# Kernel optimization log

Hardware: AMD Instinct MI355X
Metric: run time of the kernel (lower is better)

The kernel has to match this reference:

```python
import jax, jax.numpy as jnp
import numpy as np

N0, N1, NB = 247808, 22528, 2048
E0, E1 = 225280, 20480
C = 256
EW = 600000

def setup_inputs() -> dict:
    key = jax.random.key(0)
    ks = jax.random.split(key, 16)
    s = 1.0 / np.sqrt(C)
    return {
        "x": jax.random.normal(ks[0], (N0, C), dtype=jnp.float32),
        "src0": jax.random.randint(ks[1], (E0,), 0, N0),
        "dst0": jax.random.randint(ks[2], (E0,), 0, N1),
        "eid0": jax.random.randint(ks[3], (E0,), 0, EW),
        "src1": jax.random.randint(ks[4], (E1,), 0, N1),
        "dst1": jax.random.randint(ks[5], (E1,), 0, NB),
        "eid1": jax.random.randint(ks[6], (E1,), 0, EW),
        "edge_weight": jax.random.uniform(ks[7], (EW,), dtype=jnp.float32),
        "W_rel0": jax.random.uniform(ks[8], (C, C), jnp.float32, -s, s),
        "b0": jax.random.uniform(ks[9], (C,), jnp.float32, -s, s),
        "W_root0": jax.random.uniform(ks[10], (C, C), jnp.float32, -s, s),
        "W_rel1": jax.random.uniform(ks[11], (C, C), jnp.float32, -s, s),
        "b1": jax.random.uniform(ks[12], (C,), jnp.float32, -s, s),
        "W_root1": jax.random.uniform(ks[13], (C, C), jnp.float32, -s, s),
    }

def graph_conv(x, src, dst, ew, n_dst, W_rel, b, W_root):
    # PyG GraphConv, aggr='mean', bipartite: out_i = W_rel * mean_j(e_ji * x_j) + W_root * x_i + b
    msg = ew[:, None] * x[src]                                   # [E, C]
    agg = jax.ops.segment_sum(msg, dst, num_segments=n_dst)      # [n_dst, C]
    cnt = jax.ops.segment_sum(jnp.ones_like(ew), dst, num_segments=n_dst)
    mean = agg / jnp.maximum(cnt, 1.0)[:, None]
    return mean @ W_rel + b + x[:n_dst] @ W_root

def reference(x, src0, dst0, eid0, src1, dst1, eid1, edge_weight,
              W_rel0, b0, W_root0, W_rel1, b1, W_root1):
    h = graph_conv(x, src0, dst0, edge_weight[eid0], N1, W_rel0, b0, W_root0)
    h = jax.nn.relu(h)  # dropout is identity in eval mode
    h = graph_conv(h, src1, dst1, edge_weight[eid1], NB, W_rel1, b1, W_root1)
    return h, jax.nn.log_softmax(h, axis=1)
```

## Files before the change

### kernel.cpp

```cpp
#include <hip/hip_runtime.h>
#include <cstdint>
#include <cmath>

#define N0c 247808
#define N1c 22528
#define NBc 2048
#define E0c 225280
#define E1c 20480
#define Cc  256
#define NDST (N1c + NBc)
#define ETOT (E0c + E1c)

typedef __attribute__((ext_vector_type(8))) short short8;
typedef __attribute__((ext_vector_type(4))) float floatx4;

__device__ inline unsigned short f2bf(float f) {
    union { float f; unsigned u; } cv; cv.f = f;
    unsigned u = cv.u;
    u += 0x7fffu + ((u >> 16) & 1u);
    return (unsigned short)(u >> 16);
}

__global__ __launch_bounds__(256) void prep_kernel(
    const int* __restrict__ dst0, const int* __restrict__ dst1, int* __restrict__ cnt,
    const float* __restrict__ Wrel0, const float* __restrict__ Wroot0,
    const float* __restrict__ Wrel1, const float* __restrict__ Wroot1,
    short* __restrict__ Wp0, short* __restrict__ Wp1) {
    int b = blockIdx.x;
    if (b < ETOT / 256) {
        int e = b * 256 + threadIdx.x;
        if (e < E0c) atomicAdd(&cnt[dst0[e]], 1);
        else         atomicAdd(&cnt[N1c + dst1[e - E0c]], 1);
    } else {
        int gid = (b - ETOT / 256) * 256 + threadIdx.x;
        int lane = gid & 63;
        int kt = (gid >> 6) & 15;
        int nt = (gid >> 10) & 15;
        int layer = gid >> 14;
        const float* Wrel  = layer ? Wrel1  : Wrel0;
        const float* Wroot = layer ? Wroot1 : Wroot0;
        short* Wp = layer ? Wp1 : Wp0;
        int nn = nt * 16 + (lane & 15);
        int kb = kt * 32 + (lane >> 4) * 8;
        short8 v;
#pragma unroll
        for (int j = 0; j < 8; j++) {
            int k = kb + j;
            float f = (k < 256) ? Wrel[k * 256 + nn] : Wroot[(k - 256) * 256 + nn];
            v[j] = (short)f2bf(f);
        }
        *(short8*)(Wp + (((size_t)nt * 16 + kt) * 64 + lane) * 8) = v;
    }
}

__global__ __launch_bounds__(256) void scan_part(const int* __restrict__ in,
                                                 int* __restrict__ out,
                                                 int* __restrict__ partials) {
    __shared__ int wsum[4];
    int t = threadIdx.x, lane = t & 63, w = t >> 6;
    int base = blockIdx.x * 1024 + t * 4;
    int4 v = *(const int4*)(in + base);
    int s = v.x + v.y + v.z + v.w;
    int incl = s;
#pragma unroll
    for (int o = 1; o < 64; o <<= 1) {
        int u = __shfl_up(incl, o);
        if (lane >= o) incl += u;
    }
    if (lane == 63) wsum[w] = incl;
    __syncthreads();
    int woff = 0;
    for (int j = 0; j < w; j++) woff += wsum[j];
    int excl = woff + incl - s;
    int4 o4;
    o4.x = excl; excl += v.x;
    o4.y = excl; excl += v.y;
    o4.z = excl; excl += v.z;
    o4.w = excl; excl += v.w;
    *(int4*)(out + base) = o4;
    if (t == 255) partials[blockIdx.x] = woff + incl;
}

__global__ __launch_bounds__(256) void scan_add(int* __restrict__ off, int* __restrict__ cur,
                                                const int* __restrict__ partials) {
    __shared__ int pfx_s;
    int t = threadIdx.x;
    if (t < 32) {
        int v = (t < NDST / 1024) ? partials[t] : 0;
        int incl = v;
#pragma unroll
        for (int o = 1; o < 32; o <<= 1) {
            int u = __shfl_up(incl, o);
            if (t >= o) incl += u;
        }
        if (t == (int)blockIdx.x) pfx_s = incl - v;
        if (blockIdx.x == 0 && t == NDST / 1024 - 1) off[NDST] = incl;
    }
    __syncthreads();
    int p = pfx_s;
    int base = blockIdx.x * 1024 + t * 4;
    int4 v = *(const int4*)(off + base);
    v.x += p; v.y += p; v.z += p; v.w += p;
    *(int4*)(off + base) = v;
    *(int4*)(cur + base) = v;
}

__global__ void fill_both(const int* __restrict__ src0, const int* __restrict__ dst0,
                          const int* __restrict__ eid0,
                          const int* __restrict__ src1, const int* __restrict__ dst1,
                          const int* __restrict__ eid1,
                          const float* __restrict__ ew,
                          int* __restrict__ cur, int* __restrict__ srcs,
                          float* __restrict__ wsr) {
    int e = blockIdx.x * blockDim.x + threadIdx.x;
    if (e < E0c) {
        int p = atomicAdd(&cur[dst0[e]], 1);
        srcs[p] = src0[e];
        wsr[p] = ew[eid0[e]];
    } else if (e < ETOT) {
        int i = e - E0c;
        int p = atomicAdd(&cur[N1c + dst1[i]], 1);
        srcs[p] = src1[i];
        wsr[p] = ew[eid1[i]];
    }
}

template <bool ROOT>
__global__ __launch_bounds__(256) void gather_mean_bf16(const float* __restrict__ feat,
                                                        const int* __restrict__ off,
                                                        const int* __restrict__ srcs,
                                                        const float* __restrict__ wsr,
                                                        short* __restrict__ outA,
                                                        int baseRow, int nrows) {
    int wid  = (blockIdx.x * blockDim.x + threadIdx.x) >> 6;
    int lane = threadIdx.x & 63;
    if (wid >= nrows) return;
    int crow = baseRow + wid;
    int s = off[crow], e = off[crow + 1];
    float4 acc = make_float4(0.f, 0.f, 0.f, 0.f);
    int i = s;
    for (; i + 3 < e; i += 4) {
        int   s0 = srcs[i],     s1 = srcs[i + 1], s2 = srcs[i + 2], s3 = srcs[i + 3];
        float w0 = wsr[i],      w1 = wsr[i + 1],  w2 = wsr[i + 2],  w3 = wsr[i + 3];
        float4 v0 = ((const float4*)(feat + (size_t)s0 * Cc))[lane];
        float4 v1 = ((const float4*)(feat + (size_t)s1 * Cc))[lane];
        float4 v2 = ((const float4*)(feat + (size_t)s2 * Cc))[lane];
        float4 v3 = ((const float4*)(feat + (size_t)s3 * Cc))[lane];
        acc.x += w0 * v0.x + w1 * v1.x + w2 * v2.x + w3 * v3.x;
        acc.y += w0 * v0.y + w1 * v1.y + w2 * v2.y + w3 * v3.y;
        acc.z += w0 * v0.z + w1 * v1.z + w2 * v2.z + w3 * v3.z;
        acc.w += w0 * v0.w + w1 * v1.w + w2 * v2.w + w3 * v3.w;
    }
    for (; i < e; i++) {
        int sid = srcs[i];
        float w = wsr[i];
        float4 v = ((const float4*)(feat + (size_t)sid * Cc))[lane];
        acc.x += w * v.x; acc.y += w * v.y; acc.z += w * v.z; acc.w += w * v.w;
    }
    float inv = 1.0f / fmaxf((float)(e - s), 1.0f);
    ushort4 o;
    o.x = f2bf(acc.x * inv); o.y = f2bf(acc.y * inv);
    o.z = f2bf(acc.z * inv); o.w = f2bf(acc.w * inv);
    *(ushort4*)(outA + (size_t)wid * 512 + lane * 4) = o;
    if (ROOT) {
        float4 r = ((const float4*)(feat + (size_t)crow * Cc))[lane];
        ushort4 ro;
        ro.x = f2bf(r.x); ro.y = f2bf(r.y); ro.z = f2bf(r.z); ro.w = f2bf(r.w);
        *(ushort4*)(outA + (size_t)wid * 512 + 256 + lane * 4) = ro;
    }
}

template <bool RELU, bool EXTRA, bool SMAX>
__global__ __launch_bounds__(256) void gemm_mfma(const short* __restrict__ A,
                                                 const short* __restrict__ Wp,
                                                 const float* __restrict__ bias,
                                                 float* __restrict__ out,
                                                 short* __restrict__ extra,
                                                 float* __restrict__ out1) {
    __shared__ short As[32 * 520];
    int t = threadIdx.x;
    int base = blockIdx.x * 32;
#pragma unroll
    for (int it = 0; it < 8; it++) {
        int idx = it * 256 + t;
        int row = idx >> 6, c = idx & 63;
        short8 v = *(const short8*)(A + (size_t)(base + row) * 512 + c * 8);
        *(short8*)(&As[row * 520 + c * 8]) = v;
    }
    __syncthreads();

    int lane = t & 63, w = t >> 6;
    int l15 = lane & 15, lq = lane >> 4;
    floatx4 acc[2][4];
#pragma unroll
    for (int rt = 0; rt < 2; rt++)
#pragma unroll
        for (int ct = 0; ct < 4; ct++) acc[rt][ct] = (floatx4){0.f, 0.f, 0.f, 0.f};

    for (int kt = 0; kt < 16; kt++) {
        short8 a0 = *(const short8*)(&As[l15 * 520 + kt * 32 + lq * 8]);
        short8 a1 = *(const short8*)(&As[(16 + l15) * 520 + kt * 32 + lq * 8]);
#pragma unroll
        for (int ct = 0; ct < 4; ct++) {
            int nt = w * 4 + ct;
            short8 b = *(const short8*)(Wp + (((size_t)nt * 16 + kt) * 64 + lane) * 8);
            acc[0][ct] = __builtin_amdgcn_mfma_f32_16x16x32_bf16(a0, b, acc[0][ct], 0, 0, 0);
            acc[1][ct] = __builtin_amdgcn_mfma_f32_16x16x32_bf16(a1, b, acc[1][ct], 0, 0, 0);
        }
    }

    float* Ls = (float*)As;
    if (SMAX) __syncthreads();

#pragma unroll
    for (int rt = 0; rt < 2; rt++)
#pragma unroll
        for (int ct = 0; ct < 4; ct++) {
            int col = (w * 4 + ct) * 16 + l15;
            float bv = bias[col];
#pragma unroll
            for (int r = 0; r < 4; r++) {
                int rl = rt * 16 + lq * 4 + r;
                int row = base + rl;
                float val = acc[rt][ct][r] + bv;
                if (RELU) val = fmaxf(val, 0.f);
                out[(size_t)row * Cc + col] = val;
                if (EXTRA) {
                    if (row < NBc) extra[(size_t)row * 512 + 256 + col] = (short)f2bf(val);
                }
                if (SMAX) Ls[rl * 260 + col] = val;
            }
        }

    if (SMAX) {
        __syncthreads();
        for (int rr = 0; rr < 8; rr++) {
            int rl = w * 8 + rr;
            float4 v = *(const float4*)(Ls + rl * 260 + lane * 4);
            float m = fmaxf(fmaxf(v.x, v.y), fmaxf(v.z, v.w));
#pragma unroll
            for (int o = 32; o; o >>= 1) m = fmaxf(m, __shfl_xor(m, o));
            float s = expf(v.x - m) + expf(v.y - m) + expf(v.z - m) + expf(v.w - m);
#pragma unroll
            for (int o = 32; o; o >>= 1) s += __shfl_xor(s, o);
            float lse = m + logf(s);
            float4 o4;
            o4.x = v.x - lse; o4.y = v.y - lse; o4.z = v.z - lse; o4.w = v.w - lse;
            *(float4*)(out1 + (size_t)(base + rl) * Cc + lane * 4) = o4;
        }
    }
}

extern "C" void kernel_launch(void* const* d_in, const int* in_sizes, int n_in,
                              void* d_out, int out_size, void* d_ws, size_t ws_size,
                              hipStream_t stream) {
    const float* x     = (const float*)d_in[0];
    const int*   src0  = (const int*)d_in[1];
    const int*   dst0  = (const int*)d_in[2];
    const int*   eid0  = (const int*)d_in[3];
    const int*   src1  = (const int*)d_in[4];
    const int*   dst1  = (const int*)d_in[5];
    const int*   eid1  = (const int*)d_in[6];
    const float* ew    = (const float*)d_in[7];
    const float* Wrel0 = (const float*)d_in[8];
    const float* b0    = (const float*)d_in[9];
    const float* Wroot0= (const float*)d_in[10];
    const float* Wrel1 = (const float*)d_in[11];
    const float* b1    = (const float*)d_in[12];
    const float* Wroot1= (const float*)d_in[13];

    char* wsb = (char*)d_ws;
    size_t o = 0;
    auto alloc = [&](size_t bytes) { void* p = wsb + o; o += (bytes + 15) & ~(size_t)15; return p; };
    int*   off   = (int*)  alloc((NDST + 1) * 4);
    int*   cnt   = (int*)  alloc(NDST * 4);
    int*   srcs  = (int*)  alloc(ETOT * 4);
    float* wsr   = (float*)alloc(ETOT * 4);
    int*   parts = (int*)  alloc(64 * 4);
    short* Wp0   = (short*)alloc(16 * 16 * 64 * 8 * 2);
    short* Wp1   = (short*)alloc(16 * 16 * 64 * 8 * 2);
    short* A0    = (short*)alloc((size_t)N1c * 512 * 2);
    short* A1    = (short*)alloc((size_t)NBc * 512 * 2);
    float* h     = (float*)alloc((size_t)N1c * Cc * 4);

    hipMemsetAsync(cnt, 0, NDST * sizeof(int), stream);
    prep_kernel<<<ETOT / 256 + 128, 256, 0, stream>>>(dst0, dst1, cnt,
                                                      Wrel0, Wroot0, Wrel1, Wroot1, Wp0, Wp1);
    scan_part<<<NDST / 1024, 256, 0, stream>>>(cnt, off, parts);
    scan_add<<<NDST / 1024, 256, 0, stream>>>(off, cnt, parts);
    fill_both<<<ETOT / 256, 256, 0, stream>>>(src0, dst0, eid0, src1, dst1, eid1,
                                              ew, cnt, srcs, wsr);

    gather_mean_bf16<true><<<(N1c * 64) / 256, 256, 0, stream>>>(x, off, srcs, wsr, A0, 0, N1c);
    gemm_mfma<true, true, false><<<N1c / 32, 256, 0, stream>>>(A0, Wp0, b0, h, A1, nullptr);

    gather_mean_bf16<false><<<(NBc * 64) / 256, 256, 0, stream>>>(h, off, srcs, wsr, A1, N1c, NBc);
    float* out2 = (float*)d_out;
    gemm_mfma<false, false, true><<<NBc / 32, 256, 0, stream>>>(A1, Wp1, b1, out2, nullptr,
                                                                out2 + (size_t)NBc * Cc);
}
```

Baseline: 442.5 us.

## Fuse neighbor gather-mean into MFMA GEMMs and store hidden layer as bf16

Each layer's gather-mean aggregation and root-row load now write straight into the GEMM's shared-memory A tile, so the bf16 A0/A1 staging buffers and their global round trip are gone. Two kernel launches are removed. The hidden activation is kept only as bf16, which halves the layer-2 gather traffic but makes layer 2 read bf16-rounded h instead of fp32. Edge source and weight are packed into one int2 record so each edge needs one load. The risk is that gather latency inside the GEMM blocks is now serialized with the MFMA phase, with fewer resident blocks available to hide it.

```diff
diff --git a/kernel.cpp b/kernel.cpp
--- a/kernel.cpp
+++ b/kernel.cpp
@@ -19,6 +19,10 @@
     unsigned u = cv.u;
     u += 0x7fffu + ((u >> 16) & 1u);
     return (unsigned short)(u >> 16);
+}
+__device__ inline float bf2f(unsigned short u) {
+    union { unsigned u; float f; } cv; cv.u = ((unsigned)u) << 16;
+    return cv.f;
 }
 
 __global__ __launch_bounds__(256) void prep_kernel(
@@ -110,93 +114,71 @@
                           const int* __restrict__ src1, const int* __restrict__ dst1,
                           const int* __restrict__ eid1,
                           const float* __restrict__ ew,
-                          int* __restrict__ cur, int* __restrict__ srcs,
-                          float* __restrict__ wsr) {
+                          int* __restrict__ cur, int2* __restrict__ recs) {
     int e = blockIdx.x * blockDim.x + threadIdx.x;
     if (e < E0c) {
         int p = atomicAdd(&cur[dst0[e]], 1);
-        srcs[p] = src0[e];
-        wsr[p] = ew[eid0[e]];
+        recs[p] = make_int2(src0[e], __float_as_int(ew[eid0[e]]));
     } else if (e < ETOT) {
         int i = e - E0c;
         int p = atomicAdd(&cur[N1c + dst1[i]], 1);
-        srcs[p] = src1[i];
-        wsr[p] = ew[eid1[i]];
-    }
-}
-
-template <bool ROOT>
-__global__ __launch_bounds__(256) void gather_mean_bf16(const float* __restrict__ feat,
-                                                        const int* __restrict__ off,
-                                                        const int* __restrict__ srcs,
-                                                        const float* __restrict__ wsr,
-                                                        short* __restrict__ outA,
-                                                        int baseRow, int nrows) {
-    int wid  = (blockIdx.x * blockDim.x + threadIdx.x) >> 6;
-    int lane = threadIdx.x & 63;
-    if (wid >= nrows) return;
-    int crow = baseRow + wid;
-    int s = off[crow], e = off[crow + 1];
-    float4 acc = make_float4(0.f, 0.f, 0.f, 0.f);
-    int i = s;
-    for (; i + 3 < e; i += 4) {
-        int   s0 = srcs[i],     s1 = srcs[i + 1], s2 = srcs[i + 2], s3 = srcs[i + 3];
-        float w0 = wsr[i],      w1 = wsr[i + 1],  w2 = wsr[i + 2],  w3 = wsr[i + 3];
-        float4 v0 = ((const float4*)(feat + (size_t)s0 * Cc))[lane];
-        float4 v1 = ((const float4*)(feat + (size_t)s1 * Cc))[lane];
-        float4 v2 = ((const float4*)(feat + (size_t)s2 * Cc))[lane];
-        float4 v3 = ((const float4*)(feat + (size_t)s3 * Cc))[lane];
-        acc.x += w0 * v0.x + w1 * v1.x + w2 * v2.x + w3 * v3.x;
-        acc.y += w0 * v0.y + w1 * v1.y + w2 * v2.y + w3 * v3.y;
-        acc.z += w0 * v0.z + w1 * v1.z + w2 * v2.z + w3 * v3.z;
-        acc.w += w0 * v0.w + w1 * v1.w + w2 * v2.w + w3 * v3.w;
-    }
-    for (; i < e; i++) {
-        int sid = srcs[i];
-        float w = wsr[i];
-        float4 v = ((const float4*)(feat + (size_t)sid * Cc))[lane];
-        acc.x += w * v.x; acc.y += w * v.y; acc.z += w * v.z; acc.w += w * v.w;
-    }
-    float inv = 1.0f / fmaxf((float)(e - s), 1.0f);
-    ushort4 o;
-    o.x = f2bf(acc.x * inv); o.y = f2bf(acc.y * inv);
-    o.z = f2bf(acc.z * inv); o.w = f2bf(acc.w * inv);
-    *(ushort4*)(outA + (size_t)wid * 512 + lane * 4) = o;
-    if (ROOT) {
-        float4 r = ((const float4*)(feat + (size_t)crow * Cc))[lane];
+        recs[p] = make_int2(src1[i], __float_as_int(ew[eid1[i]]));
+    }
+}
+
+__global__ __launch_bounds__(256) void gemm0_fused(const float* __restrict__ x,
+                                                   const int* __restrict__ off,
+                                                   const int2* __restrict__ recs,
+                                                   const short* __restrict__ Wp,
+                                                   const float* __restrict__ bias,
+                                                   short* __restrict__ hb) {
+    __shared__ short As[32 * 520];
+    int t = threadIdx.x, lane = t & 63, w = t >> 6;
+    int base = blockIdx.x * 32;
+
+    for (int r = 0; r < 8; r++) {
+        int rl = w * 8 + r;
+        int row = base + rl;
+        int s = off[row], e = off[row + 1];
+        float4 acc = make_float4(0.f, 0.f, 0.f, 0.f);
+        int i = s;
+        for (; i + 3 < e; i += 4) {
+            int2 r0 = recs[i], r1 = recs[i + 1], r2 = recs[i + 2], r3 = recs[i + 3];
+            float w0 = __int_as_float(r0.y), w1 = __int_as_float(r1.y);
+            float w2 = __int_as_float(r2.y), w3 = __int_as_float(r3.y);
+            float4 v0 = ((const float4*)(x + (size_t)r0.x * Cc))[lane];
+            float4 v1 = ((const float4*)(x + (size_t)r1.x * Cc))[lane];
+            float4 v2 = ((const float4*)(x + (size_t)r2.x * Cc))[lane];
+            float4 v3 = ((const float4*)(x + (size_t)r3.x * Cc))[lane];
+            acc.x += w0 * v0.x + w1 * v1.x + w2 * v2.x + w3 * v3.x;
+            acc.y += w0 * v0.y + w1 * v1.y + w2 * v2.y + w3 * v3.y;
+            acc.z += w0 * v0.z + w1 * v1.z + w2 * v2.z + w3 * v3.z;
+            acc.w += w0 * v0.w + w1 * v1.w + w2 * v2.w + w3 * v3.w;
+        }
+        for (; i < e; i++) {
+            int2 rc = recs[i];
+            float ww = __int_as_float(rc.y);
+            float4 v = ((const float4*)(x + (size_t)rc.x * Cc))[lane];
+            acc.x += ww * v.x; acc.y += ww * v.y; acc.z += ww * v.z; acc.w += ww * v.w;
+        }
+        float inv = 1.0f / fmaxf((float)(e - s), 1.0f);
+        ushort4 m;
+        m.x = f2bf(acc.x * inv); m.y = f2bf(acc.y * inv);
+        m.z = f2bf(acc.z * inv); m.w = f2bf(acc.w * inv);
+        *(ushort4*)(&As[rl * 520 + lane * 4]) = m;
+        float4 rv = ((const float4*)(x + (size_t)row * Cc))[lane];
         ushort4 ro;
-        ro.x = f2bf(r.x); ro.y = f2bf(r.y); ro.z = f2bf(r.z); ro.w = f2bf(r.w);
-        *(ushort4*)(outA + (size_t)wid * 512 + 256 + lane * 4) = ro;
-    }
-}
-
-template <bool RELU, bool EXTRA, bool SMAX>
-__global__ __launch_bounds__(256) void gemm_mfma(const short* __restrict__ A,
-                                                 const short* __restrict__ Wp,
-                                                 const float* __restrict__ bias,
-                                                 float* __restrict__ out,
-                                                 short* __restrict__ extra,
-                                                 float* __restrict__ out1) {
-    __shared__ short As[32 * 520];
-    int t = threadIdx.x;
-    int base = blockIdx.x * 32;
-#pragma unroll
-    for (int it = 0; it < 8; it++) {
-        int idx = it * 256 + t;
-        int row = idx >> 6, c = idx & 63;
-        short8 v = *(const short8*)(A + (size_t)(base + row) * 512 + c * 8);
-        *(short8*)(&As[row * 520 + c * 8]) = v;
-    }
-    __syncthreads();
-
-    int lane = t & 63, w = t >> 6;
+        ro.x = f2bf(rv.x); ro.y = f2bf(rv.y); ro.z = f2bf(rv.z); ro.w = f2bf(rv.w);
+        *(ushort4*)(&As[rl * 520 + 256 + lane * 4]) = ro;
+    }
+    __syncthreads();
+
     int l15 = lane & 15, lq = lane >> 4;
     floatx4 acc[2][4];
 #pragma unroll
     for (int rt = 0; rt < 2; rt++)
 #pragma unroll
         for (int ct = 0; ct < 4; ct++) acc[rt][ct] = (floatx4){0.f, 0.f, 0.f, 0.f};
-
     for (int kt = 0; kt < 16; kt++) {
         short8 a0 = *(const short8*)(&As[l15 * 520 + kt * 32 + lq * 8]);
         short8 a1 = *(const short8*)(&As[(16 + l15) * 520 + kt * 32 + lq * 8]);
@@ -208,10 +190,9 @@
             acc[1][ct] = __builtin_amdgcn_mfma_f32_16x16x32_bf16(a1, b, acc[1][ct], 0, 0, 0);
         }
     }
-
-    float* Ls = (float*)As;
-    if (SMAX) __syncthreads();
-
+    __syncthreads();
+
+    short* Os = As;
 #pragma unroll
     for (int rt = 0; rt < 2; rt++)
 #pragma unroll
@@ -221,33 +202,115 @@
 #pragma unroll
             for (int r = 0; r < 4; r++) {
                 int rl = rt * 16 + lq * 4 + r;
-                int row = base + rl;
-                float val = acc[rt][ct][r] + bv;
-                if (RELU) val = fmaxf(val, 0.f);
-                out[(size_t)row * Cc + col] = val;
-                if (EXTRA) {
-                    if (row < NBc) extra[(size_t)row * 512 + 256 + col] = (short)f2bf(val);
-                }
-                if (SMAX) Ls[rl * 260 + col] = val;
+                float val = fmaxf(acc[rt][ct][r] + bv, 0.f);
+                Os[rl * 260 + col] = (short)f2bf(val);
             }
         }
-
-    if (SMAX) {
-        __syncthreads();
-        for (int rr = 0; rr < 8; rr++) {
-            int rl = w * 8 + rr;
-            float4 v = *(const float4*)(Ls + rl * 260 + lane * 4);
-            float m = fmaxf(fmaxf(v.x, v.y), fmaxf(v.z, v.w));
-#pragma unroll
-            for (int o = 32; o; o >>= 1) m = fmaxf(m, __shfl_xor(m, o));
-            float s = expf(v.x - m) + expf(v.y - m) + expf(v.z - m) + expf(v.w - m);
-#pragma unroll
-            for (int o = 32; o; o >>= 1) s += __shfl_xor(s, o);
-            float lse = m + logf(s);
-            float4 o4;
-            o4.x = v.x - lse; o4.y = v.y - lse; o4.z = v.z - lse; o4.w = v.w - lse;
-            *(float4*)(out1 + (size_t)(base + rl) * Cc + lane * 4) = o4;
-        }
+    __syncthreads();
+#pragma unroll
+    for (int it = 0; it < 8; it++) {
+        int idx = it * 256 + t;
+        int row = idx >> 6, c = idx & 63;
+        ushort4 v = *(const ushort4*)(&Os[row * 260 + c * 4]);
+        *(ushort4*)(hb + (size_t)(base + row) * Cc + c * 4) = v;
+    }
+}
+
+__global__ __launch_bounds__(256) void gemm1_fused(const short* __restrict__ hb,
+                                                   const int* __restrict__ off,
+                                                   const int2* __restrict__ recs,
+                                                   const short* __restrict__ Wp,
+                                                   const float* __restrict__ bias,
+                                                   float* __restrict__ out0,
+                                                   float* __restrict__ out1) {
+    __shared__ short As[32 * 520];
+    int t = threadIdx.x, lane = t & 63, w = t >> 6;
+    int base = blockIdx.x * 32;
+
+    for (int r = 0; r < 8; r++) {
+        int rl = w * 8 + r;
+        int row = base + rl;
+        int crow = N1c + row;
+        int s = off[crow], e = off[crow + 1];
+        float4 acc = make_float4(0.f, 0.f, 0.f, 0.f);
+        int i = s;
+        for (; i + 3 < e; i += 4) {
+            int2 r0 = recs[i], r1 = recs[i + 1], r2 = recs[i + 2], r3 = recs[i + 3];
+            float w0 = __int_as_float(r0.y), w1 = __int_as_float(r1.y);
+            float w2 = __int_as_float(r2.y), w3 = __int_as_float(r3.y);
+            ushort4 h0 = ((const ushort4*)(hb + (size_t)r0.x * Cc))[lane];
+            ushort4 h1 = ((const ushort4*)(hb + (size_t)r1.x * Cc))[lane];
+            ushort4 h2 = ((const ushort4*)(hb + (size_t)r2.x * Cc))[lane];
+            ushort4 h3 = ((const ushort4*)(hb + (size_t)r3.x * Cc))[lane];
+            acc.x += w0 * bf2f(h0.x) + w1 * bf2f(h1.x) + w2 * bf2f(h2.x) + w3 * bf2f(h3.x);
+            acc.y += w0 * bf2f(h0.y) + w1 * bf2f(h1.y) + w2 * bf2f(h2.y) + w3 * bf2f(h3.y);
+            acc.z += w0 * bf2f(h0.z) + w1 * bf2f(h1.z) + w2 * bf2f(h2.z) + w3 * bf2f(h3.z);
+            acc.w += w0 * bf2f(h0.w) + w1 * bf2f(h1.w) + w2 * bf2f(h2.w) + w3 * bf2f(h3.w);
+        }
+        for (; i < e; i++) {
+            int2 rc = recs[i];
+            float ww = __int_as_float(rc.y);
+            ushort4 hv = ((const ushort4*)(hb + (size_t)rc.x * Cc))[lane];
+            acc.x += ww * bf2f(hv.x); acc.y += ww * bf2f(hv.y);
+            acc.z += ww * bf2f(hv.z); acc.w += ww * bf2f(hv.w);
+        }
+        float inv = 1.0f / fmaxf((float)(e - s), 1.0f);
+        ushort4 m;
+        m.x = f2bf(acc.x * inv); m.y = f2bf(acc.y * inv);
+        m.z = f2bf(acc.z * inv); m.w = f2bf(acc.w * inv);
+        *(ushort4*)(&As[rl * 520 + lane * 4]) = m;
+        ushort4 ro = ((const ushort4*)(hb + (size_t)row * Cc))[lane];
+        *(ushort4*)(&As[rl * 520 + 256 + lane * 4]) = ro;
+    }
+    __syncthreads();
+
+    int l15 = lane & 15, lq = lane >> 4;
+    floatx4 acc[2][4];
+#pragma unroll
+    for (int rt = 0; rt < 2; rt++)
+#pragma unroll
+        for (int ct = 0; ct < 4; ct++) acc[rt][ct] = (floatx4){0.f, 0.f, 0.f, 0.f};
+    for (int kt = 0; kt < 16; kt++) {
+        short8 a0 = *(const short8*)(&As[l15 * 520 + kt * 32 + lq * 8]);
+        short8 a1 = *(const short8*)(&As[(16 + l15) * 520 + kt * 32 + lq * 8]);
+#pragma unroll
+        for (int ct = 0; ct < 4; ct++) {
+            int nt = w * 4 + ct;
+            short8 b = *(const short8*)(Wp + (((size_t)nt * 16 + kt) * 64 + lane) * 8);
+            acc[0][ct] = __builtin_amdgcn_mfma_f32_16x16x32_bf16(a0, b, acc[0][ct], 0, 0, 0);
+            acc[1][ct] = __builtin_amdgcn_mfma_f32_16x16x32_bf16(a1, b, acc[1][ct], 0, 0, 0);
+        }
+    }
+    __syncthreads();
+
+    float* Ls = (float*)As;
+#pragma unroll
+    for (int rt = 0; rt < 2; rt++)
+#pragma unroll
+        for (int ct = 0; ct < 4; ct++) {
+            int col = (w * 4 + ct) * 16 + l15;
+            float bv = bias[col];
+#pragma unroll
+            for (int r = 0; r < 4; r++) {
+                int rl = rt * 16 + lq * 4 + r;
+                Ls[rl * 260 + col] = acc[rt][ct][r] + bv;
+            }
+        }
+    __syncthreads();
+    for (int rr = 0; rr < 8; rr++) {
+        int rl = w * 8 + rr;
+        float4 v = *(const float4*)(Ls + rl * 260 + lane * 4);
+        *(float4*)(out0 + (size_t)(base + rl) * Cc + lane * 4) = v;
+        float m = fmaxf(fmaxf(v.x, v.y), fmaxf(v.z, v.w));
+#pragma unroll
+        for (int o = 32; o; o >>= 1) m = fmaxf(m, __shfl_xor(m, o));
+        float s = expf(v.x - m) + expf(v.y - m) + expf(v.z - m) + expf(v.w - m);
+#pragma unroll
+        for (int o = 32; o; o >>= 1) s += __shfl_xor(s, o);
+        float lse = m + logf(s);
+        float4 o4;
+        o4.x = v.x - lse; o4.y = v.y - lse; o4.z = v.z - lse; o4.w = v.w - lse;
+        *(float4*)(out1 + (size_t)(base + rl) * Cc + lane * 4) = o4;
     }
 }
 
@@ -274,14 +337,11 @@
     auto alloc = [&](size_t bytes) { void* p = wsb + o; o += (bytes + 15) & ~(size_t)15; return p; };
     int*   off   = (int*)  alloc((NDST + 1) * 4);
     int*   cnt   = (int*)  alloc(NDST * 4);
-    int*   srcs  = (int*)  alloc(ETOT * 4);
-    float* wsr   = (float*)alloc(ETOT * 4);
+    int2*  recs  = (int2*) alloc(ETOT * 8);
     int*   parts = (int*)  alloc(64 * 4);
     short* Wp0   = (short*)alloc(16 * 16 * 64 * 8 * 2);
     short* Wp1   = (short*)alloc(16 * 16 * 64 * 8 * 2);
-    short* A0    = (short*)alloc((size_t)N1c * 512 * 2);
-    short* A1    = (short*)alloc((size_t)NBc * 512 * 2);
-    float* h     = (float*)alloc((size_t)N1c * Cc * 4);
+    short* hb    = (short*)alloc((size_t)N1c * Cc * 2);
 
     hipMemsetAsync(cnt, 0, NDST * sizeof(int), stream);
     prep_kernel<<<ETOT / 256 + 128, 256, 0, stream>>>(dst0, dst1, cnt,
@@ -289,13 +349,10 @@
     scan_part<<<NDST / 1024, 256, 0, stream>>>(cnt, off, parts);
     scan_add<<<NDST / 1024, 256, 0, stream>>>(off, cnt, parts);
     fill_both<<<ETOT / 256, 256, 0, stream>>>(src0, dst0, eid0, src1, dst1, eid1,
-                                              ew, cnt, srcs, wsr);
-
-    gather_mean_bf16<true><<<(N1c * 64) / 256, 256, 0, stream>>>(x, off, srcs, wsr, A0, 0, N1c);
-    gemm_mfma<true, true, false><<<N1c / 32, 256, 0, stream>>>(A0, Wp0, b0, h, A1, nullptr);
-
-    gather_mean_bf16<false><<<(NBc * 64) / 256, 256, 0, stream>>>(h, off, srcs, wsr, A1, N1c, NBc);
+                                              ew, cnt, recs);
+
+    gemm0_fused<<<N1c / 32, 256, 0, stream>>>(x, off, recs, Wp0, b0, hb);
     float* out2 = (float*)d_out;
-    gemm_mfma<false, false, true><<<NBc / 32, 256, 0, stream>>>(A1, Wp1, b1, out2, nullptr,
-                                                                out2 + (size_t)NBc * Cc);
-}
+    gemm1_fused<<<NBc / 32, 256, 0, stream>>>(hb, off, recs, Wp1, b1,
+                                              out2, out2 + (size_t)NBc * Cc);
+}
```

Measured after the change: 443.9 us (median of 2 runs). Within noise of the previous version (+0.3%).
